# Kernel optimization log

Measured on AMD Instinct MI355X. Metric: run time of the kernel, lower is better.

## Reference

```python
import jax, jax.numpy as jnp
import numpy as np

N_NODES = 100000
N_EDGES = 1600000
N_PAIRS = 200000
IN_C, HID_C, OUT_C = 128, 128, 64


def setup_inputs() -> dict:
    key = jax.random.key(0)
    ks = jax.random.split(key, 10)
    x = jax.random.normal(ks[0], (N_NODES, IN_C), dtype=jnp.float32)
    edge_index = jax.random.randint(ks[1], (2, N_EDGES), 0, N_NODES, dtype=jnp.int64)
    node_i = jax.random.randint(ks[2], (N_PAIRS,), 0, N_NODES, dtype=jnp.int64)
    node_j = jax.random.randint(ks[3], (N_PAIRS,), 0, N_NODES, dtype=jnp.int64)
    def glorot(k, fan_in, fan_out):
        s = jnp.sqrt(6.0 / (fan_in + fan_out))
        return jax.random.uniform(k, (fan_in, fan_out), jnp.float32, -s, s)
    W1 = glorot(ks[4], IN_C, HID_C)
    b1 = jnp.zeros((HID_C,), jnp.float32)
    W2 = glorot(ks[5], HID_C, HID_C)
    b2 = jnp.zeros((HID_C,), jnp.float32)
    W3 = glorot(ks[6], HID_C, OUT_C)
    b3 = jnp.zeros((OUT_C,), jnp.float32)
    return {"x": x, "edge_index": edge_index, "node_i": node_i, "node_j": node_j,
            "W1": W1, "b1": b1, "W2": W2, "b2": b2, "W3": W3, "b3": b3}


def _gcn_layer(h, src, dst, deg_inv, w_e, W, b):
    # h: [N, Cin] -> linear then symmetric-normalized aggregation (with self loops)
    h = h @ W  # [N, Cout]
    msg = h[src] * w_e[:, None]  # [E, Cout] gather + edge weight
    agg = jax.ops.segment_sum(msg, dst, num_segments=N_NODES)
    agg = agg + h * deg_inv[:, None]  # self-loop term: h_i / deg_i
    return agg + b


def reference(x, edge_index, node_i, node_j, W1, b1, W2, b2, W3, b3):
    src, dst = edge_index[0], edge_index[1]
    # GCN normalization with self loops: deg_i = 1 + in-degree
    ones = jnp.ones((N_EDGES,), jnp.float32)
    deg = jax.ops.segment_sum(ones, dst, num_segments=N_NODES) + 1.0
    dinv_sqrt = jax.lax.rsqrt(deg)
    deg_inv = 1.0 / deg
    w_e = dinv_sqrt[src] * dinv_sqrt[dst]  # [E]

    h = _gcn_layer(x, src, dst, deg_inv, w_e, W1, b1)
    h = jax.nn.relu(h)  # dropout is identity in eval mode
    h = _gcn_layer(h, src, dst, deg_inv, w_e, W2, b2)
    h = jax.nn.relu(h)
    h = _gcn_layer(h, src, dst, deg_inv, w_e, W3, b3)

    # dot-product link decode (decode_type=None)
    return jnp.sum(h[node_i] * h[node_j], axis=-1)  # [N_PAIRS]
```

## Files before the change

kernel.cpp:

```cpp
#include <hip/hip_runtime.h>

#define NN 100000
#define NNP 100032
#define NE 1600000
#define NP 200000
#define NBKT 782
#define BCAP 3072
#define BKB 4096

typedef short s16x8 __attribute__((ext_vector_type(8)));
typedef float f32x4 __attribute__((ext_vector_type(4)));
typedef float f32x2 __attribute__((ext_vector_type(2)));

__device__ __forceinline__ unsigned short f2bf(float f) {
  unsigned int u = __float_as_uint(f);
  u += 0x7fffu + ((u >> 16) & 1u);
  return (unsigned short)(u >> 16);
}

__device__ __forceinline__ void pkadd(f32x2& a, uint u) {
  f32x2 v;
  v.x = __uint_as_float(u << 16);
  v.y = __uint_as_float(u & 0xffff0000u);
  asm("v_pk_add_f32 %0, %0, %1" : "+v"(a) : "v"(v));
}

__device__ __forceinline__ void rowadd(uint4 v, f32x2* a) {
  pkadd(a[0], v.x);
  pkadd(a[1], v.y);
  pkadd(a[2], v.z);
  pkadd(a[3], v.w);
}

template <int RSH>
__device__ __forceinline__ void gath(const int* __restrict__ col,
                                     const char* __restrict__ Tb, int s,
                                     int tend, uint co, f32x2* acc) {
  const int d = tend - s;
  const int nfull = d >> 3;
  const int rem = d & 7;
  int e = s;
  int c[8];
#pragma unroll
  for (int j = 0; j < 8; ++j) c[j] = col[e + j];
#pragma unroll 1
  for (int it = 0; it < nfull; ++it) {
    uint4 v0 = *(const uint4*)(Tb + (((uint)c[0] << RSH) | co));
    uint4 v1 = *(const uint4*)(Tb + (((uint)c[1] << RSH) | co));
    uint4 v2 = *(const uint4*)(Tb + (((uint)c[2] << RSH) | co));
    uint4 v3 = *(const uint4*)(Tb + (((uint)c[3] << RSH) | co));
    uint4 v4 = *(const uint4*)(Tb + (((uint)c[4] << RSH) | co));
    uint4 v5 = *(const uint4*)(Tb + (((uint)c[5] << RSH) | co));
    uint4 v6 = *(const uint4*)(Tb + (((uint)c[6] << RSH) | co));
    uint4 v7 = *(const uint4*)(Tb + (((uint)c[7] << RSH) | co));
    e += 8;
#pragma unroll
    for (int j = 0; j < 8; ++j) c[j] = col[e + j];
    rowadd(v0, acc);
    rowadd(v1, acc);
    rowadd(v2, acc);
    rowadd(v3, acc);
    rowadd(v4, acc);
    rowadd(v5, acc);
    rowadd(v6, acc);
    rowadd(v7, acc);
  }
  if (rem) {
#pragma unroll
    for (int j = 0; j < 8; ++j) c[j] = (j < rem) ? c[j] : NN;
    uint4 v0 = *(const uint4*)(Tb + (((uint)c[0] << RSH) | co));
    uint4 v1 = *(const uint4*)(Tb + (((uint)c[1] << RSH) | co));
    uint4 v2 = *(const uint4*)(Tb + (((uint)c[2] << RSH) | co));
    uint4 v3 = *(const uint4*)(Tb + (((uint)c[3] << RSH) | co));
    uint4 v4 = *(const uint4*)(Tb + (((uint)c[4] << RSH) | co));
    uint4 v5 = *(const uint4*)(Tb + (((uint)c[5] << RSH) | co));
    uint4 v6 = *(const uint4*)(Tb + (((uint)c[6] << RSH) | co));
    uint4 v7 = *(const uint4*)(Tb + (((uint)c[7] << RSH) | co));
    rowadd(v0, acc);
    rowadd(v1, acc);
    rowadd(v2, acc);
    rowadd(v3, acc);
    rowadd(v4, acc);
    rowadd(v5, acc);
    rowadd(v6, acc);
    rowadd(v7, acc);
  }
}

template <int NT>
__device__ __forceinline__ void prepw_dev(const float* __restrict__ W,
                                          uint* __restrict__ Wt, int tid) {
  constexpr int COUT = NT * 16;
  if (tid >= 4 * NT * 64) return;
  int lane = tid & 63, comb = tid >> 6;
  int ks = comb / NT, tl = comb % NT;
  int q = lane >> 4, n = lane & 15;
  uint w[4];
#pragma unroll
  for (int jj = 0; jj < 4; ++jj) {
    int k0 = ks * 32 + q * 8 + 2 * jj;
    uint lo = f2bf(W[k0 * COUT + tl * 16 + n]);
    uint hi = f2bf(W[(k0 + 1) * COUT + tl * 16 + n]);
    w[jj] = lo | (hi << 16);
  }
  ((uint4*)Wt)[comb * 64 + lane] = make_uint4(w[0], w[1], w[2], w[3]);
}

__global__ __launch_bounds__(256) void k_setup(const float* __restrict__ W1,
                                               const float* __restrict__ W2,
                                               const float* __restrict__ W3,
                                               uint* __restrict__ Wt1,
                                               uint* __restrict__ Wt2,
                                               uint* __restrict__ Wt3,
                                               int* __restrict__ gcur) {
  int b = blockIdx.x, t = threadIdx.x;
  if (b < 4) {
    int i = b * 256 + t;
    if (i < 1024) gcur[i] = 0;
  } else if (b < 12) {
    prepw_dev<8>(W1, Wt1, (b - 4) * 256 + t);
  } else if (b < 20) {
    prepw_dev<8>(W2, Wt2, (b - 12) * 256 + t);
  } else {
    prepw_dev<4>(W3, Wt3, (b - 20) * 256 + t);
  }
}

__global__ __launch_bounds__(256) void k_bucket(const int* __restrict__ ei,
                                                int* __restrict__ gcur,
                                                int* __restrict__ aux) {
  __shared__ int cnt[1024];
  __shared__ int scn[1024];
  __shared__ int cur[1024];
  __shared__ int sc[256];
  __shared__ int sorted[BKB];
  __shared__ unsigned short sbkt[BKB];
  const int t = threadIdx.x;
  const int base = blockIdx.x * BKB;

  for (int i = t; i < 1024; i += 256) cnt[i] = 0;
  __syncthreads();

  int pk[16], bk[16];
#pragma unroll
  for (int i = 0; i < 16; ++i) {
    int e = base + t + 256 * i;
    if (e < NE) {
      int src = ei[e], dst = ei[NE + e];
      bk[i] = dst >> 7;
      pk[i] = src | ((dst & 127) << 17);
      atomicAdd(&cnt[bk[i]], 1);
    } else {
      bk[i] = -1;
    }
  }
  __syncthreads();

  int s0 = cnt[4 * t], s1 = cnt[4 * t + 1], s2 = cnt[4 * t + 2], s3 = cnt[4 * t + 3];
  int local = s0 + s1 + s2 + s3;
  sc[t] = local;
  __syncthreads();
  for (int off = 1; off < 256; off <<= 1) {
    int a = (t >= off) ? sc[t - off] : 0;
    __syncthreads();
    sc[t] += a;
    __syncthreads();
  }
  int b0 = sc[t] - local;
  scn[4 * t] = b0;
  scn[4 * t + 1] = b0 + s0;
  scn[4 * t + 2] = b0 + s0 + s1;
  scn[4 * t + 3] = b0 + s0 + s1 + s2;
  cur[4 * t] = scn[4 * t];
  cur[4 * t + 1] = scn[4 * t + 1];
  cur[4 * t + 2] = scn[4 * t + 2];
  cur[4 * t + 3] = scn[4 * t + 3];
  __syncthreads();
  const int tot = sc[255];

#pragma unroll
  for (int i = 0; i < 16; ++i) {
    if (bk[i] >= 0) {
      int pos = atomicAdd(&cur[bk[i]], 1);
      sorted[pos] = pk[i];
      sbkt[pos] = (unsigned short)bk[i];
    }
  }
  __syncthreads();

  for (int b = t; b < 1024; b += 256) {
    int c = cnt[b];
    if (c > 0) cur[b] = b * BCAP + atomicAdd(&gcur[b], c);
  }
  __syncthreads();

  for (int k = t; k < tot; k += 256) {
    int b = sbkt[k];
    aux[cur[b] + (k - scn[b])] = sorted[k];
  }
}

__global__ __launch_bounds__(256) void k_csr(const int* __restrict__ gcur,
                                             const int* __restrict__ aux,
                                             int* __restrict__ row_ptr,
                                             float* __restrict__ dinv,
                                             int* __restrict__ col) {
  __shared__ int red[256];
  __shared__ int c[128];
  __shared__ int cur[128];
  const int b = blockIdx.x, t = threadIdx.x;
  int p = 0;
  for (int i = t; i < b; i += 256) p += gcur[i];
  red[t] = p;
  if (t < 128) c[t] = 0;
  __syncthreads();
  for (int off = 128; off > 0; off >>= 1) {
    if (t < off) red[t] += red[t + off];
    __syncthreads();
  }
  const int base = red[0];
  const int m = gcur[b];
  const int* a = aux + (size_t)b * BCAP;
  __syncthreads();
  for (int k = t; k < m; k += 256) atomicAdd(&c[a[k] >> 17], 1);
  __syncthreads();
  int val = (t < 128) ? c[t] : 0;
  red[t] = val;
  __syncthreads();
  for (int off = 1; off < 128; off <<= 1) {
    int add = (t >= off && t < 128) ? red[t - off] : 0;
    __syncthreads();
    if (t < 128) red[t] += add;
    __syncthreads();
  }
  if (t < 128) {
    int excl = red[t] - val + base;
    int node = b * 128 + t;
    if (node < NN) {
      row_ptr[node] = excl;
      dinv[node] = rsqrtf((float)(val + 1));
      cur[t] = excl;
    }
  }
  if (b == NBKT - 1 && t == 0) row_ptr[NN] = base + m;
  __syncthreads();
  for (int k = t; k < m; k += 256) {
    int pk2 = a[k];
    int pos = atomicAdd(&cur[pk2 >> 17], 1);
    col[pos] = pk2 & 0x1FFFF;
  }
}

__global__ __launch_bounds__(256) void k_gemm1(const float* __restrict__ A,
                                               const uint* __restrict__ Wt,
                                               const float* __restrict__ dinv,
                                               unsigned short* __restrict__ T) {
  constexpr int NT = 8, COUT = 128;
  __shared__ __align__(16) uint Wlds[4 * NT * 64 * 4];
  __shared__ __align__(16) unsigned short Obuf[64 * COUT];
  const int t = threadIdx.x;
  {
    const uint4* src = (const uint4*)Wt;
    uint4* dst = (uint4*)Wlds;
    for (int i = t; i < 4 * NT * 64; i += 256) dst[i] = src[i];
  }
  __syncthreads();

  const int wv = t >> 6, lane = t & 63;
  const int n = lane & 15, quad = lane >> 4;
  const int rbase = blockIdx.x * 64 + wv * 16;

  union AB { uint4 u; s16x8 s; };
  AB a[4];
  {
    int row = rbase + n;
    if (row >= NN) row = NN - 1;
    const float* ap = A + (size_t)row * 128;
#pragma unroll
    for (int ks = 0; ks < 4; ++ks) {
      float4 v0 = *(const float4*)(ap + ks * 32 + quad * 8);
      float4 v1 = *(const float4*)(ap + ks * 32 + quad * 8 + 4);
      a[ks].u.x = (uint)f2bf(v0.x) | ((uint)f2bf(v0.y) << 16);
      a[ks].u.y = (uint)f2bf(v0.z) | ((uint)f2bf(v0.w) << 16);
      a[ks].u.z = (uint)f2bf(v1.x) | ((uint)f2bf(v1.y) << 16);
      a[ks].u.w = (uint)f2bf(v1.z) | ((uint)f2bf(v1.w) << 16);
    }
  }

  f32x4 acc[NT];
#pragma unroll
  for (int tl = 0; tl < NT; ++tl) acc[tl] = (f32x4){0.f, 0.f, 0.f, 0.f};

#pragma unroll
  for (int ks = 0; ks < 4; ++ks) {
#pragma unroll
    for (int tl = 0; tl < NT; ++tl) {
      AB b;
      b.u = *(const uint4*)&Wlds[((ks * NT + tl) * 64 + lane) * 4];
      acc[tl] = __builtin_amdgcn_mfma_f32_16x16x32_bf16(a[ks].s, b.s, acc[tl], 0, 0, 0);
    }
  }

  float4 dv = *(const float4*)(dinv + rbase + quad * 4);
  float dvv[4] = {dv.x, dv.y, dv.z, dv.w};
  unsigned short* ob = Obuf + wv * 16 * COUT;
#pragma unroll
  for (int tl = 0; tl < NT; ++tl)
#pragma unroll
    for (int r = 0; r < 4; ++r)
      ob[(quad * 4 + r) * COUT + tl * 16 + n] = f2bf(acc[tl][r] * dvv[r]);

  uint4* gdst = (uint4*)(T + (size_t)rbase * COUT);
#pragma unroll
  for (int i = 0; i < 4; ++i) {
    int off16 = i * 64 + lane;
    int lrow = (off16 * 8) / COUT;
    uint4 v = make_uint4(0u, 0u, 0u, 0u);
    if (rbase + lrow < NN) v = *(const uint4*)&ob[off16 * 8];
    gdst[off16] = v;
  }
}

template <int COUT>
__global__ __launch_bounds__(256) void k_gg(const int* __restrict__ row_ptr,
                                            const int* __restrict__ col,
                                            const uint4* __restrict__ T4,
                                            const float* __restrict__ dinv,
                                            const float* __restrict__ bias,
                                            const uint4* __restrict__ Wt,
                                            unsigned short* __restrict__ Tout) {
  constexpr int NT = COUT / 16;
  constexpr int TLW = NT / 4;
  constexpr int OSTR = COUT + 8;
  __shared__ __align__(16) uint4 Alds[16 * 17];
  const int t = threadIdx.x, wv = t >> 6, lane = t & 63;
  const int nbase = blockIdx.x * 16;
  const int q = lane >> 4, cl = lane & 15;

  const int node = nbase + wv * 4 + q;
  int s = 0, tend = 0;
  if (node < NN) {
    s = row_ptr[node];
    tend = row_ptr[node + 1];
  }
  const char* Tb = (const char*)T4;
  const uint co = (uint)cl << 4;
  f32x2 acc[4];
  acc[0] = (f32x2){0.f, 0.f};
  acc[1] = (f32x2){0.f, 0.f};
  acc[2] = (f32x2){0.f, 0.f};
  acc[3] = (f32x2){0.f, 0.f};
  rowadd(*(const uint4*)(Tb + (((uint)node << 8) | co)), acc);
  gath<8>(col, Tb, s, tend, co, acc);

  {
    float dv = dinv[node];
    float4 b0 = *(const float4*)&bias[cl * 8];
    float4 b1 = *(const float4*)&bias[cl * 8 + 4];
    float r0 = fmaxf(fmaf(dv, acc[0].x, b0.x), 0.f);
    float r1 = fmaxf(fmaf(dv, acc[0].y, b0.y), 0.f);
    float r2 = fmaxf(fmaf(dv, acc[1].x, b0.z), 0.f);
    float r3 = fmaxf(fmaf(dv, acc[1].y, b0.w), 0.f);
    float r4 = fmaxf(fmaf(dv, acc[2].x, b1.x), 0.f);
    float r5 = fmaxf(fmaf(dv, acc[2].y, b1.y), 0.f);
    float r6 = fmaxf(fmaf(dv, acc[3].x, b1.z), 0.f);
    float r7 = fmaxf(fmaf(dv, acc[3].y, b1.w), 0.f);
    uint4 o;
    o.x = (uint)f2bf(r0) | ((uint)f2bf(r1) << 16);
    o.y = (uint)f2bf(r2) | ((uint)f2bf(r3) << 16);
    o.z = (uint)f2bf(r4) | ((uint)f2bf(r5) << 16);
    o.w = (uint)f2bf(r6) | ((uint)f2bf(r7) << 16);
    Alds[(wv * 4 + q) * 17 + cl] = o;
  }
  __syncthreads();

  const int n = lane & 15, quad = lane >> 4;
  union AB { uint4 u; s16x8 s; };
  AB a[4];
#pragma unroll
  for (int ks = 0; ks < 4; ++ks) a[ks].u = Alds[n * 17 + ks * 4 + quad];
  f32x4 acc2[TLW];
#pragma unroll
  for (int j = 0; j < TLW; ++j) acc2[j] = (f32x4){0.f, 0.f, 0.f, 0.f};
#pragma unroll
  for (int ks = 0; ks < 4; ++ks) {
#pragma unroll
    for (int j = 0; j < TLW; ++j) {
      int tl = wv * TLW + j;
      AB b;
      b.u = Wt[(ks * NT + tl) * 64 + lane];
      acc2[j] = __builtin_amdgcn_mfma_f32_16x16x32_bf16(a[ks].s, b.s, acc2[j], 0, 0, 0);
    }
  }
  __syncthreads();

  unsigned short* Obuf = (unsigned short*)Alds;
  float4 dv4 = *(const float4*)(dinv + nbase + quad * 4);
  float dvv[4] = {dv4.x, dv4.y, dv4.z, dv4.w};
#pragma unroll
  for (int j = 0; j < TLW; ++j) {
    int tl = wv * TLW + j;
#pragma unroll
    for (int r = 0; r < 4; ++r)
      Obuf[(quad * 4 + r) * OSTR + tl * 16 + n] = f2bf(acc2[j][r] * dvv[r]);
  }
  __syncthreads();

  if constexpr (COUT == 128) {
    int row = t >> 4, c16 = t & 15;
    uint4 v = make_uint4(0u, 0u, 0u, 0u);
    if (nbase + row < NN) v = *(const uint4*)&Obuf[row * OSTR + c16 * 8];
    ((uint4*)(Tout + (size_t)nbase * COUT))[row * 16 + c16] = v;
  } else {
    if (t < 128) {
      int row = t >> 3, c16 = t & 7;
      uint4 v = make_uint4(0u, 0u, 0u, 0u);
      if (nbase + row < NN) v = *(const uint4*)&Obuf[row * OSTR + c16 * 8];
      ((uint4*)(Tout + (size_t)nbase * COUT))[row * 8 + c16] = v;
    }
  }
}

__global__ __launch_bounds__(256) void k_gather3(const int* __restrict__ row_ptr,
                                                 const int* __restrict__ col,
                                                 const uint4* __restrict__ T4,
                                                 const float* __restrict__ dinv,
                                                 const float* __restrict__ b3,
                                                 uint4* __restrict__ G3) {
  const int wid = (blockIdx.x * 256 + threadIdx.x) >> 6;
  const int lane = threadIdx.x & 63;
  const int g = lane >> 3, cl = lane & 7;
  const int node = wid * 8 + g;
  if (node >= NN) return;
  int s = row_ptr[node], tend = row_ptr[node + 1];
  const char* Tb = (const char*)T4;
  const uint co = (uint)cl << 4;
  f32x2 acc[4];
  acc[0] = (f32x2){0.f, 0.f};
  acc[1] = (f32x2){0.f, 0.f};
  acc[2] = (f32x2){0.f, 0.f};
  acc[3] = (f32x2){0.f, 0.f};
  rowadd(*(const uint4*)(Tb + (((uint)node << 7) | co)), acc);
  gath<7>(col, Tb, s, tend, co, acc);
  float dv = dinv[node];
  float4 bb0 = *(const float4*)&b3[cl * 8];
  float4 bb1 = *(const float4*)&b3[cl * 8 + 4];
  float h0 = fmaf(dv, acc[0].x, bb0.x);
  float h1 = fmaf(dv, acc[0].y, bb0.y);
  float h2 = fmaf(dv, acc[1].x, bb0.z);
  float h3 = fmaf(dv, acc[1].y, bb0.w);
  float h4 = fmaf(dv, acc[2].x, bb1.x);
  float h5 = fmaf(dv, acc[2].y, bb1.y);
  float h6 = fmaf(dv, acc[3].x, bb1.z);
  float h7 = fmaf(dv, acc[3].y, bb1.w);
  uint4 o;
  o.x = (uint)f2bf(h0) | ((uint)f2bf(h1) << 16);
  o.y = (uint)f2bf(h2) | ((uint)f2bf(h3) << 16);
  o.z = (uint)f2bf(h4) | ((uint)f2bf(h5) << 16);
  o.w = (uint)f2bf(h6) | ((uint)f2bf(h7) << 16);
  G3[(size_t)node * 8 + cl] = o;
}

__global__ __launch_bounds__(256) void k_decode(const int* __restrict__ ni,
                                                const int* __restrict__ nj,
                                                const uint2* __restrict__ G3,
                                                float* __restrict__ out) {
  int p = blockIdx.x * 16 + (threadIdx.x >> 4);
  int cl = threadIdx.x & 15;
  int i = ni[p], j = nj[p];
  uint2 ui = G3[(size_t)i * 16 + cl];
  uint2 uj = G3[(size_t)j * 16 + cl];
  float gi0 = __uint_as_float(ui.x << 16), gi1 = __uint_as_float(ui.x & 0xffff0000u);
  float gi2 = __uint_as_float(ui.y << 16), gi3 = __uint_as_float(ui.y & 0xffff0000u);
  float gj0 = __uint_as_float(uj.x << 16), gj1 = __uint_as_float(uj.x & 0xffff0000u);
  float gj2 = __uint_as_float(uj.y << 16), gj3 = __uint_as_float(uj.y & 0xffff0000u);
  float v = gi0 * gj0 + gi1 * gj1 + gi2 * gj2 + gi3 * gj3;
  v += __shfl_xor(v, 1, 64);
  v += __shfl_xor(v, 2, 64);
  v += __shfl_xor(v, 4, 64);
  v += __shfl_xor(v, 8, 64);
  if (cl == 0) out[p] = v;
}

extern "C" void kernel_launch(void* const* d_in, const int* in_sizes, int n_in,
                              void* d_out, int out_size, void* d_ws, size_t ws_size,
                              hipStream_t stream) {
  const float* x  = (const float*)d_in[0];
  const int*   ei = (const int*)d_in[1];
  const int*   ni = (const int*)d_in[2];
  const int*   nj = (const int*)d_in[3];
  const float* W1 = (const float*)d_in[4];
  const float* b1 = (const float*)d_in[5];
  const float* W2 = (const float*)d_in[6];
  const float* b2 = (const float*)d_in[7];
  const float* W3 = (const float*)d_in[8];
  const float* b3 = (const float*)d_in[9];
  float* out = (float*)d_out;

  float* dinv    = (float*)d_ws;
  int*   row_ptr = (int*)(dinv + 102400);
  int*   gcur    = row_ptr + 102400;
  int*   col     = gcur + 1024;
  uint*  Wt1     = (uint*)(col + NE);
  uint*  Wt2     = Wt1 + 8192;
  uint*  Wt3     = Wt2 + 8192;
  uint*  Tbf     = Wt3 + 4096;
  uint*  T2      = Tbf + (size_t)NNP * 64;
  uint*  G3      = T2 + (size_t)NNP * 64;
  int*   aux     = (int*)G3;

  k_setup<<<24, 256, 0, stream>>>(W1, W2, W3, Wt1, Wt2, Wt3, gcur);
  k_bucket<<<(NE + BKB - 1) / BKB, 256, 0, stream>>>(ei, gcur, aux);
  k_csr<<<NBKT, 256, 0, stream>>>(gcur, aux, row_ptr, dinv, col);

  const int GB = NNP / 64;
  const int FB = NNP / 16;
  const int GATB = (NN + 31) / 32;

  k_gemm1<<<GB, 256, 0, stream>>>(x, Wt1, dinv, (unsigned short*)Tbf);
  k_gg<128><<<FB, 256, 0, stream>>>(row_ptr, col, (const uint4*)Tbf, dinv, b1,
                                    (const uint4*)Wt2, (unsigned short*)T2);
  k_gg<64><<<FB, 256, 0, stream>>>(row_ptr, col, (const uint4*)T2, dinv, b2,
                                   (const uint4*)Wt3, (unsigned short*)Tbf);
  k_gather3<<<GATB, 256, 0, stream>>>(row_ptr, col, (const uint4*)Tbf, dinv, b3,
                                      (uint4*)G3);
  k_decode<<<NP / 16, 256, 0, stream>>>(ni, nj, (const uint2*)G3, out);
}
```

Before: 303.0 us.

## Parameterize gather unroll depth, use nontemporal edge loads, memset counters

The gather helper now takes its batch depth as a template parameter, and the layer-2/3 fused kernel uses a depth of 10 instead of 8 to keep more row loads in flight. Edge index loads in the bucketing kernel become nontemporal. Zeroing of the bucket counters moves from the setup kernel to a hipMemsetAsync, which adds an extra operation on the stream. The deeper unroll raises register pressure and can lower occupancy.

```diff
diff --git a/kernel.cpp b/kernel.cpp
--- a/kernel.cpp
+++ b/kernel.cpp
@@ -32,58 +32,38 @@
   pkadd(a[3], v.w);
 }
 
-template <int RSH>
+template <int RSH, int D>
 __device__ __forceinline__ void gath(const int* __restrict__ col,
                                      const char* __restrict__ Tb, int s,
                                      int tend, uint co, f32x2* acc) {
   const int d = tend - s;
-  const int nfull = d >> 3;
-  const int rem = d & 7;
+  const int nfull = d / D;
+  const int rem = d - nfull * D;
   int e = s;
-  int c[8];
-#pragma unroll
-  for (int j = 0; j < 8; ++j) c[j] = col[e + j];
+  int c[D];
+#pragma unroll
+  for (int j = 0; j < D; ++j) c[j] = col[e + j];
 #pragma unroll 1
   for (int it = 0; it < nfull; ++it) {
-    uint4 v0 = *(const uint4*)(Tb + (((uint)c[0] << RSH) | co));
-    uint4 v1 = *(const uint4*)(Tb + (((uint)c[1] << RSH) | co));
-    uint4 v2 = *(const uint4*)(Tb + (((uint)c[2] << RSH) | co));
-    uint4 v3 = *(const uint4*)(Tb + (((uint)c[3] << RSH) | co));
-    uint4 v4 = *(const uint4*)(Tb + (((uint)c[4] << RSH) | co));
-    uint4 v5 = *(const uint4*)(Tb + (((uint)c[5] << RSH) | co));
-    uint4 v6 = *(const uint4*)(Tb + (((uint)c[6] << RSH) | co));
-    uint4 v7 = *(const uint4*)(Tb + (((uint)c[7] << RSH) | co));
-    e += 8;
-#pragma unroll
-    for (int j = 0; j < 8; ++j) c[j] = col[e + j];
-    rowadd(v0, acc);
-    rowadd(v1, acc);
-    rowadd(v2, acc);
-    rowadd(v3, acc);
-    rowadd(v4, acc);
-    rowadd(v5, acc);
-    rowadd(v6, acc);
-    rowadd(v7, acc);
+    uint4 v[D];
+#pragma unroll
+    for (int j = 0; j < D; ++j)
+      v[j] = *(const uint4*)(Tb + (((uint)c[j] << RSH) | co));
+    e += D;
+#pragma unroll
+    for (int j = 0; j < D; ++j) c[j] = col[e + j];
+#pragma unroll
+    for (int j = 0; j < D; ++j) rowadd(v[j], acc);
   }
   if (rem) {
 #pragma unroll
-    for (int j = 0; j < 8; ++j) c[j] = (j < rem) ? c[j] : NN;
-    uint4 v0 = *(const uint4*)(Tb + (((uint)c[0] << RSH) | co));
-    uint4 v1 = *(const uint4*)(Tb + (((uint)c[1] << RSH) | co));
-    uint4 v2 = *(const uint4*)(Tb + (((uint)c[2] << RSH) | co));
-    uint4 v3 = *(const uint4*)(Tb + (((uint)c[3] << RSH) | co));
-    uint4 v4 = *(const uint4*)(Tb + (((uint)c[4] << RSH) | co));
-    uint4 v5 = *(const uint4*)(Tb + (((uint)c[5] << RSH) | co));
-    uint4 v6 = *(const uint4*)(Tb + (((uint)c[6] << RSH) | co));
-    uint4 v7 = *(const uint4*)(Tb + (((uint)c[7] << RSH) | co));
-    rowadd(v0, acc);
-    rowadd(v1, acc);
-    rowadd(v2, acc);
-    rowadd(v3, acc);
-    rowadd(v4, acc);
-    rowadd(v5, acc);
-    rowadd(v6, acc);
-    rowadd(v7, acc);
+    for (int j = 0; j < D; ++j) c[j] = (j < rem) ? c[j] : NN;
+    uint4 v[D];
+#pragma unroll
+    for (int j = 0; j < D; ++j)
+      v[j] = *(const uint4*)(Tb + (((uint)c[j] << RSH) | co));
+#pragma unroll
+    for (int j = 0; j < D; ++j) rowadd(v[j], acc);
   }
 }
 
@@ -111,18 +91,14 @@
                                                const float* __restrict__ W3,
                                                uint* __restrict__ Wt1,
                                                uint* __restrict__ Wt2,
-                                               uint* __restrict__ Wt3,
-                                               int* __restrict__ gcur) {
+                                               uint* __restrict__ Wt3) {
   int b = blockIdx.x, t = threadIdx.x;
-  if (b < 4) {
-    int i = b * 256 + t;
-    if (i < 1024) gcur[i] = 0;
-  } else if (b < 12) {
-    prepw_dev<8>(W1, Wt1, (b - 4) * 256 + t);
-  } else if (b < 20) {
-    prepw_dev<8>(W2, Wt2, (b - 12) * 256 + t);
+  if (b < 8) {
+    prepw_dev<8>(W1, Wt1, b * 256 + t);
+  } else if (b < 16) {
+    prepw_dev<8>(W2, Wt2, (b - 8) * 256 + t);
   } else {
-    prepw_dev<4>(W3, Wt3, (b - 20) * 256 + t);
+    prepw_dev<4>(W3, Wt3, (b - 16) * 256 + t);
   }
 }
 
@@ -146,7 +122,8 @@
   for (int i = 0; i < 16; ++i) {
     int e = base + t + 256 * i;
     if (e < NE) {
-      int src = ei[e], dst = ei[NE + e];
+      int src = __builtin_nontemporal_load(&ei[e]);
+      int dst = __builtin_nontemporal_load(&ei[NE + e]);
       bk[i] = dst >> 7;
       pk[i] = src | ((dst & 127) << 17);
       atomicAdd(&cnt[bk[i]], 1);
@@ -351,7 +328,7 @@
   acc[2] = (f32x2){0.f, 0.f};
   acc[3] = (f32x2){0.f, 0.f};
   rowadd(*(const uint4*)(Tb + (((uint)node << 8) | co)), acc);
-  gath<8>(col, Tb, s, tend, co, acc);
+  gath<8, 10>(col, Tb, s, tend, co, acc);
 
   {
     float dv = dinv[node];
@@ -441,7 +418,7 @@
   acc[2] = (f32x2){0.f, 0.f};
   acc[3] = (f32x2){0.f, 0.f};
   rowadd(*(const uint4*)(Tb + (((uint)node << 7) | co)), acc);
-  gath<7>(col, Tb, s, tend, co, acc);
+  gath<7, 8>(col, Tb, s, tend, co, acc);
   float dv = dinv[node];
   float4 bb0 = *(const float4*)&b3[cl * 8];
   float4 bb1 = *(const float4*)&b3[cl * 8 + 4];
@@ -509,7 +486,8 @@
   uint*  G3      = T2 + (size_t)NNP * 64;
   int*   aux     = (int*)G3;
 
-  k_setup<<<24, 256, 0, stream>>>(W1, W2, W3, Wt1, Wt2, Wt3, gcur);
+  hipMemsetAsync(gcur, 0, 1024 * sizeof(int), stream);
+  k_setup<<<20, 256, 0, stream>>>(W1, W2, W3, Wt1, Wt2, Wt3);
   k_bucket<<<(NE + BKB - 1) / BKB, 256, 0, stream>>>(ei, gcur, aux);
   k_csr<<<NBKT, 256, 0, stream>>>(gcur, aux, row_ptr, dinv, col);
 
```

New measurement: 311.4 us. 1.03x slower.
